# Kernel tuning notes

Measured on AMD Instinct MI355X. Metric: run time of the kernel, lower is better.

## Reference

```python
import jax, jax.numpy as jnp
import numpy as np

B, D = 4096, 512
STEPS = 50
LR, B1, B2, EPS = 0.01, 0.9, 0.999, 1e-8  # torch.optim.Adam defaults with lr=0.01


def setup_inputs() -> dict:
    key = jax.random.key(0)
    k1, k2, k3, k4 = jax.random.split(key, 4)
    s = jax.random.normal(k1, (B, D), dtype=jnp.float32)
    target_confidence = jax.random.uniform(k2, (B, 1), dtype=jnp.float32)
    # nn.Linear(style_dim, 1) init: U(-1/sqrt(D), 1/sqrt(D))
    lim = 1.0 / np.sqrt(D)
    W = jax.random.uniform(k3, (1, D), dtype=jnp.float32, minval=-lim, maxval=lim)
    b = jax.random.uniform(k4, (1,), dtype=jnp.float32, minval=-lim, maxval=lim)
    return {"s": s, "target_confidence": target_confidence, "W": W, "b": b}


def reference(s, target_confidence, W, b):
    # loss(x) = mse(sigmoid(x W^T + b), t) + l1(x, s); grad taken w.r.t. x only.
    def loss_fn(x):
        p = jax.nn.sigmoid(x @ W.T + b)                      # [B, 1]
        mse = jnp.mean((p - target_confidence) ** 2)
        d = x - s
        # stop_gradient(sign) so d|d|/dx = sign(d), with sign(0) = 0 (matches torch l1_loss subgradient)
        l1 = jnp.mean(jax.lax.stop_gradient(jnp.sign(d)) * d)
        return mse + l1

    grad_fn = jax.grad(loss_fn)

    def adam_step(carry, _):
        x, m, v, t = carry
        g = grad_fn(x)
        t = t + 1.0
        m = B1 * m + (1.0 - B1) * g
        v = B2 * v + (1.0 - B2) * g * g
        m_hat = m / (1.0 - B1 ** t)
        v_hat = v / (1.0 - B2 ** t)
        x = x - LR * m_hat / (jnp.sqrt(v_hat) + EPS)
        return (x, m, v, t), None

    init = (s, jnp.zeros_like(s), jnp.zeros_like(s), jnp.float32(0.0))
    (adjusted_s, _, _, _), _ = jax.lax.scan(adam_step, init, None, length=STEPS)
    return adjusted_s
```

## Files before the change

### kernel.cpp

```cpp
#include <hip/hip_runtime.h>

#define B_ 4096
#define D_ 512
#define STEPS_ 50

struct BcTab { float An[STEPS_]; };

#define DPP_ADD(x, ctrl) \
    ((x) + __int_as_float(__builtin_amdgcn_update_dpp( \
        0, __float_as_int(x), (ctrl), 0xf, 0xf, true)))

__device__ __forceinline__ float wave64_sum(float x) {
    x = DPP_ADD(x, 0x111);
    x = DPP_ADD(x, 0x112);
    x = DPP_ADD(x, 0x114);
    x = DPP_ADD(x, 0x118);
    x = DPP_ADD(x, 0x142);
    x = DPP_ADD(x, 0x143);
    return __int_as_float(__builtin_amdgcn_readlane(__float_as_int(x), 63));
}

__device__ __forceinline__ float sgn_l1(float d) {
    return __uint_as_float((__float_as_uint(d) & 0x80000000u) | 0x35000000u);
}

__device__ __forceinline__ float coef_from_z(float z, float t) {
    const float e = __expf(-z);
    const float q = __builtin_amdgcn_rcpf(1.0f + e);
    return (q - t) * (e * (q * q));
}

__global__ __launch_bounds__(64, 1) void adam_rows_kernel(
    const float* __restrict__ s,
    const float* __restrict__ tgt,
    const float* __restrict__ W,
    const float* __restrict__ bias_p,
    float* __restrict__ out,
    const BcTab bc)
{
    const int lane = threadIdx.x;
    const int r0 = blockIdx.x * 2;
    const int r1 = r0 + 1;

    const float4* s0 = (const float4*)(s + (size_t)r0 * D_);
    const float4* s1 = (const float4*)(s + (size_t)r1 * D_);
    const float4* W4 = (const float4*)W;

    float4 sa0 = s0[lane], sb0 = s0[lane + 64];
    float4 sa1 = s1[lane], sb1 = s1[lane + 64];
    float4 wa  = W4[lane], wb  = W4[lane + 64];
    const float t0 = tgt[r0], t1 = tgt[r1];
    const float b  = bias_p[0];

    const float c_mse = 2.0f / (float)B_;
    const float K     = (float)B_ * 0.5f;

    float2 ws[4] = {{wa.x * c_mse, wa.y * c_mse}, {wa.z * c_mse, wa.w * c_mse},
                    {wb.x * c_mse, wb.y * c_mse}, {wb.z * c_mse, wb.w * c_mse}};
    float2 ss0[4] = {{sa0.x, sa0.y}, {sa0.z, sa0.w}, {sb0.x, sb0.y}, {sb0.z, sb0.w}};
    float2 ss1[4] = {{sa1.x, sa1.y}, {sa1.z, sa1.w}, {sb1.x, sb1.y}, {sb1.z, sb1.w}};
    float2 dl0[4], dl1[4], M0[4], M1[4], V0[4], V1[4];

    float za0 = 0.0f, za1 = 0.0f;
#pragma unroll
    for (int j = 0; j < 4; ++j) {
        za0 = fmaf(ss0[j].x, ws[j].x, za0); za0 = fmaf(ss0[j].y, ws[j].y, za0);
        za1 = fmaf(ss1[j].x, ws[j].x, za1); za1 = fmaf(ss1[j].y, ws[j].y, za1);
    }
    const float zb0 = fmaf(K, wave64_sum(za0), b);
    const float zb1 = fmaf(K, wave64_sum(za1), b);

    float du0, du1;

    {
        const float c0 = coef_from_z(zb0, t0);
        const float c1 = coef_from_z(zb1, t1);
        const float An = bc.An[0];
        float a0 = 0.0f, a1 = 0.0f;
#pragma unroll
        for (int j = 0; j < 4; ++j) {
#pragma unroll
            for (int h = 0; h < 2; ++h) {
                float* w_  = h ? &ws[j].y  : &ws[j].x;
                float* m0_ = h ? &M0[j].y  : &M0[j].x;
                float* v0_ = h ? &V0[j].y  : &V0[j].x;
                float* d0_ = h ? &dl0[j].y : &dl0[j].x;
                float* m1_ = h ? &M1[j].y  : &M1[j].x;
                float* v1_ = h ? &V1[j].y  : &V1[j].x;
                float* d1_ = h ? &dl1[j].y : &dl1[j].x;
                const float g0 = c0 * *w_;
                const float g1 = c1 * *w_;
                *m0_ = g0; *v0_ = g0 * g0;
                *m1_ = g1; *v1_ = g1 * g1;
                const float r0r = __builtin_amdgcn_rsqf(fmaxf(*v0_, 1e-37f));
                const float r1r = __builtin_amdgcn_rsqf(fmaxf(*v1_, 1e-37f));
                *d0_ = (An * *m0_) * r0r;
                *d1_ = (An * *m1_) * r1r;
                a0 = fmaf(*d0_, *w_, a0);
                a1 = fmaf(*d1_, *w_, a1);
            }
        }
        du0 = a0; du1 = a1;
    }

#pragma unroll 1
    for (int step = 1; step < STEPS_; ++step) {
        const float z0 = fmaf(K, wave64_sum(du0), zb0);
        const float z1 = fmaf(K, wave64_sum(du1), zb1);
        const float c0 = coef_from_z(z0, t0);
        const float c1 = coef_from_z(z1, t1);
        const float An = bc.An[step];

        float a0 = 0.0f, a1 = 0.0f;
#pragma unroll
        for (int j = 0; j < 4; ++j) {
#pragma unroll
            for (int h = 0; h < 2; ++h) {
                float* w_  = h ? &ws[j].y  : &ws[j].x;
                float* m0_ = h ? &M0[j].y  : &M0[j].x;
                float* v0_ = h ? &V0[j].y  : &V0[j].x;
                float* d0_ = h ? &dl0[j].y : &dl0[j].x;
                float* m1_ = h ? &M1[j].y  : &M1[j].x;
                float* v1_ = h ? &V1[j].y  : &V1[j].x;
                float* d1_ = h ? &dl1[j].y : &dl1[j].x;
                const float g0 = fmaf(c0, *w_, sgn_l1(*d0_));
                const float g1 = fmaf(c1, *w_, sgn_l1(*d1_));
                *m0_ = fmaf(0.9f, *m0_, g0);
                *m1_ = fmaf(0.9f, *m1_, g1);
                *v0_ = fmaf(0.999f, *v0_, g0 * g0);
                *v1_ = fmaf(0.999f, *v1_, g1 * g1);
                const float r0r = __builtin_amdgcn_rsqf(fmaxf(*v0_, 1e-37f));
                const float r1r = __builtin_amdgcn_rsqf(fmaxf(*v1_, 1e-37f));
                *d0_ = fmaf(An * *m0_, r0r, *d0_);
                *d1_ = fmaf(An * *m1_, r1r, *d1_);
                a0 = fmaf(*d0_, *w_, a0);
                a1 = fmaf(*d1_, *w_, a1);
            }
        }
        du0 = a0; du1 = a1;
    }

    float4 oa0 = {ss0[0].x + dl0[0].x, ss0[0].y + dl0[0].y,
                  ss0[1].x + dl0[1].x, ss0[1].y + dl0[1].y};
    float4 ob0 = {ss0[2].x + dl0[2].x, ss0[2].y + dl0[2].y,
                  ss0[3].x + dl0[3].x, ss0[3].y + dl0[3].y};
    float4 oa1 = {ss1[0].x + dl1[0].x, ss1[0].y + dl1[0].y,
                  ss1[1].x + dl1[1].x, ss1[1].y + dl1[1].y};
    float4 ob1 = {ss1[2].x + dl1[2].x, ss1[2].y + dl1[2].y,
                  ss1[3].x + dl1[3].x, ss1[3].y + dl1[3].y};
    float4* o0 = (float4*)(out + (size_t)r0 * D_);
    float4* o1 = (float4*)(out + (size_t)r1 * D_);
    o0[lane] = oa0; o0[lane + 64] = ob0;
    o1[lane] = oa1; o1[lane + 64] = ob1;
}

extern "C" void kernel_launch(void* const* d_in, const int* in_sizes, int n_in,
                              void* d_out, int out_size, void* d_ws, size_t ws_size,
                              hipStream_t stream) {
    const float* s    = (const float*)d_in[0];
    const float* tgt  = (const float*)d_in[1];
    const float* W    = (const float*)d_in[2];
    const float* bias = (const float*)d_in[3];
    float* out = (float*)d_out;

    BcTab bc;
    double p1 = 1.0, p2 = 1.0;
    for (int t = 0; t < STEPS_; ++t) {
        p1 *= 0.9; p2 *= 0.999;
        bc.An[t] = (float)((-0.001 / (1.0 - p1)) /
                           __builtin_sqrt(0.001 / (1.0 - p2)));
    }

    adam_rows_kernel<<<dim3(B_ / 2), dim3(64), 0, stream>>>(s, tgt, W, bias, out, bc);
}
```

Baseline: 96.66 us.

## Skew two-row Adam recurrence so each row's reduction overlaps the other's update

Restructures the per-step loop so row 0's cross-lane reduction and sigmoid coefficient are computed while row 1's element update runs, staggering the two serial dependency chains instead of reducing both at the top of each step. It also replaces the fmax clamp with an epsilon folded into the v initialisation, uses copysign for the L1 sign term, and reloads s at the end instead of keeping it in registers across the loop. The aim is to hide DPP reduction and transcendental latency in a single-wave, latency-bound kernel. It risks small numerical differences from the epsilon change and adds global reloads at the end.

```diff
diff --git a/kernel.cpp b/kernel.cpp
--- a/kernel.cpp
+++ b/kernel.cpp
@@ -18,10 +18,6 @@
     x = DPP_ADD(x, 0x142);
     x = DPP_ADD(x, 0x143);
     return __int_as_float(__builtin_amdgcn_readlane(__float_as_int(x), 63));
-}
-
-__device__ __forceinline__ float sgn_l1(float d) {
-    return __uint_as_float((__float_as_uint(d) & 0x80000000u) | 0x35000000u);
 }
 
 __device__ __forceinline__ float coef_from_z(float z, float t) {
@@ -46,29 +42,34 @@
     const float4* s1 = (const float4*)(s + (size_t)r1 * D_);
     const float4* W4 = (const float4*)W;
 
-    float4 sa0 = s0[lane], sb0 = s0[lane + 64];
-    float4 sa1 = s1[lane], sb1 = s1[lane + 64];
-    float4 wa  = W4[lane], wb  = W4[lane + 64];
+    const float4 wa = W4[lane], wb = W4[lane + 64];
     const float t0 = tgt[r0], t1 = tgt[r1];
     const float b  = bias_p[0];
 
-    const float c_mse = 2.0f / (float)B_;
-    const float K     = (float)B_ * 0.5f;
+    const float c_mse = 0x1p-11f;
+    const float K     = 2048.0f;
+    const float c_l1  = 0x1p-21f;
 
-    float2 ws[4] = {{wa.x * c_mse, wa.y * c_mse}, {wa.z * c_mse, wa.w * c_mse},
-                    {wb.x * c_mse, wb.y * c_mse}, {wb.z * c_mse, wb.w * c_mse}};
-    float2 ss0[4] = {{sa0.x, sa0.y}, {sa0.z, sa0.w}, {sb0.x, sb0.y}, {sb0.z, sb0.w}};
-    float2 ss1[4] = {{sa1.x, sa1.y}, {sa1.z, sa1.w}, {sb1.x, sb1.y}, {sb1.z, sb1.w}};
-    float2 dl0[4], dl1[4], M0[4], M1[4], V0[4], V1[4];
+    float ws[8] = {wa.x * c_mse, wa.y * c_mse, wa.z * c_mse, wa.w * c_mse,
+                   wb.x * c_mse, wb.y * c_mse, wb.z * c_mse, wb.w * c_mse};
 
-    float za0 = 0.0f, za1 = 0.0f;
+    float dl0[8], dl1[8], M0[8], M1[8], V0[8], V1[8];
+
+    float zb0, zb1;
+    {
+        const float4 sa0 = s0[lane], sb0 = s0[lane + 64];
+        const float4 sa1 = s1[lane], sb1 = s1[lane + 64];
+        const float e0[8] = {sa0.x, sa0.y, sa0.z, sa0.w, sb0.x, sb0.y, sb0.z, sb0.w};
+        const float e1[8] = {sa1.x, sa1.y, sa1.z, sa1.w, sb1.x, sb1.y, sb1.z, sb1.w};
+        float za0 = 0.0f, za1 = 0.0f;
 #pragma unroll
-    for (int j = 0; j < 4; ++j) {
-        za0 = fmaf(ss0[j].x, ws[j].x, za0); za0 = fmaf(ss0[j].y, ws[j].y, za0);
-        za1 = fmaf(ss1[j].x, ws[j].x, za1); za1 = fmaf(ss1[j].y, ws[j].y, za1);
+        for (int k = 0; k < 8; ++k) {
+            za0 = fmaf(e0[k], ws[k], za0);
+            za1 = fmaf(e1[k], ws[k], za1);
+        }
+        zb0 = fmaf(K, wave64_sum(za0), b);
+        zb1 = fmaf(K, wave64_sum(za1), b);
     }
-    const float zb0 = fmaf(K, wave64_sum(za0), b);
-    const float zb1 = fmaf(K, wave64_sum(za1), b);
 
     float du0, du1;
 
@@ -78,80 +79,64 @@
         const float An = bc.An[0];
         float a0 = 0.0f, a1 = 0.0f;
 #pragma unroll
-        for (int j = 0; j < 4; ++j) {
-#pragma unroll
-            for (int h = 0; h < 2; ++h) {
-                float* w_  = h ? &ws[j].y  : &ws[j].x;
-                float* m0_ = h ? &M0[j].y  : &M0[j].x;
-                float* v0_ = h ? &V0[j].y  : &V0[j].x;
-                float* d0_ = h ? &dl0[j].y : &dl0[j].x;
-                float* m1_ = h ? &M1[j].y  : &M1[j].x;
-                float* v1_ = h ? &V1[j].y  : &V1[j].x;
-                float* d1_ = h ? &dl1[j].y : &dl1[j].x;
-                const float g0 = c0 * *w_;
-                const float g1 = c1 * *w_;
-                *m0_ = g0; *v0_ = g0 * g0;
-                *m1_ = g1; *v1_ = g1 * g1;
-                const float r0r = __builtin_amdgcn_rsqf(fmaxf(*v0_, 1e-37f));
-                const float r1r = __builtin_amdgcn_rsqf(fmaxf(*v1_, 1e-37f));
-                *d0_ = (An * *m0_) * r0r;
-                *d1_ = (An * *m1_) * r1r;
-                a0 = fmaf(*d0_, *w_, a0);
-                a1 = fmaf(*d1_, *w_, a1);
-            }
+        for (int k = 0; k < 8; ++k) {
+            const float g0 = c0 * ws[k];
+            const float g1 = c1 * ws[k];
+            M0[k] = g0;  V0[k] = fmaf(g0, g0, 1e-30f);
+            M1[k] = g1;  V1[k] = fmaf(g1, g1, 1e-30f);
+            dl0[k] = (An * M0[k]) * __builtin_amdgcn_rsqf(V0[k]);
+            dl1[k] = (An * M1[k]) * __builtin_amdgcn_rsqf(V1[k]);
+            a0 = fmaf(dl0[k], ws[k], a0);
+            a1 = fmaf(dl1[k], ws[k], a1);
         }
         du0 = a0; du1 = a1;
     }
 
+    float c0 = coef_from_z(fmaf(K, wave64_sum(du0), zb0), t0);
+
 #pragma unroll 1
     for (int step = 1; step < STEPS_; ++step) {
-        const float z0 = fmaf(K, wave64_sum(du0), zb0);
-        const float z1 = fmaf(K, wave64_sum(du1), zb1);
-        const float c0 = coef_from_z(z0, t0);
-        const float c1 = coef_from_z(z1, t1);
         const float An = bc.An[step];
 
-        float a0 = 0.0f, a1 = 0.0f;
+        const float c1 = coef_from_z(fmaf(K, wave64_sum(du1), zb1), t1);
+
+        float a0 = 0.0f;
 #pragma unroll
-        for (int j = 0; j < 4; ++j) {
+        for (int k = 0; k < 8; ++k) {
+            const float g = fmaf(c0, ws[k], __builtin_copysignf(c_l1, dl0[k]));
+            M0[k] = fmaf(0.9f,   M0[k], g);
+            V0[k] = fmaf(0.999f, V0[k], g * g);
+            dl0[k] = fmaf(An * M0[k], __builtin_amdgcn_rsqf(V0[k]), dl0[k]);
+            a0 = fmaf(dl0[k], ws[k], a0);
+        }
+        du0 = a0;
+
+        c0 = coef_from_z(fmaf(K, wave64_sum(du0), zb0), t0);
+
+        float a1 = 0.0f;
 #pragma unroll
-            for (int h = 0; h < 2; ++h) {
-                float* w_  = h ? &ws[j].y  : &ws[j].x;
-                float* m0_ = h ? &M0[j].y  : &M0[j].x;
-                float* v0_ = h ? &V0[j].y  : &V0[j].x;
-                float* d0_ = h ? &dl0[j].y : &dl0[j].x;
-                float* m1_ = h ? &M1[j].y  : &M1[j].x;
-                float* v1_ = h ? &V1[j].y  : &V1[j].x;
-                float* d1_ = h ? &dl1[j].y : &dl1[j].x;
-                const float g0 = fmaf(c0, *w_, sgn_l1(*d0_));
-                const float g1 = fmaf(c1, *w_, sgn_l1(*d1_));
-                *m0_ = fmaf(0.9f, *m0_, g0);
-                *m1_ = fmaf(0.9f, *m1_, g1);
-                *v0_ = fmaf(0.999f, *v0_, g0 * g0);
-                *v1_ = fmaf(0.999f, *v1_, g1 * g1);
-                const float r0r = __builtin_amdgcn_rsqf(fmaxf(*v0_, 1e-37f));
-                const float r1r = __builtin_amdgcn_rsqf(fmaxf(*v1_, 1e-37f));
-                *d0_ = fmaf(An * *m0_, r0r, *d0_);
-                *d1_ = fmaf(An * *m1_, r1r, *d1_);
-                a0 = fmaf(*d0_, *w_, a0);
-                a1 = fmaf(*d1_, *w_, a1);
-            }
+        for (int k = 0; k < 8; ++k) {
+            const float g = fmaf(c1, ws[k], __builtin_copysignf(c_l1, dl1[k]));
+            M1[k] = fmaf(0.9f,   M1[k], g);
+            V1[k] = fmaf(0.999f, V1[k], g * g);
+            dl1[k] = fmaf(An * M1[k], __builtin_amdgcn_rsqf(V1[k]), dl1[k]);
+            a1 = fmaf(dl1[k], ws[k], a1);
         }
-        du0 = a0; du1 = a1;
+        du1 = a1;
     }
 
-    float4 oa0 = {ss0[0].x + dl0[0].x, ss0[0].y + dl0[0].y,
-                  ss0[1].x + dl0[1].x, ss0[1].y + dl0[1].y};
-    float4 ob0 = {ss0[2].x + dl0[2].x, ss0[2].y + dl0[2].y,
-                  ss0[3].x + dl0[3].x, ss0[3].y + dl0[3].y};
-    float4 oa1 = {ss1[0].x + dl1[0].x, ss1[0].y + dl1[0].y,
-                  ss1[1].x + dl1[1].x, ss1[1].y + dl1[1].y};
-    float4 ob1 = {ss1[2].x + dl1[2].x, ss1[2].y + dl1[2].y,
-                  ss1[3].x + dl1[3].x, ss1[3].y + dl1[3].y};
-    float4* o0 = (float4*)(out + (size_t)r0 * D_);
-    float4* o1 = (float4*)(out + (size_t)r1 * D_);
-    o0[lane] = oa0; o0[lane + 64] = ob0;
-    o1[lane] = oa1; o1[lane + 64] = ob1;
+    {
+        const float4 sa0 = s0[lane], sb0 = s0[lane + 64];
+        const float4 sa1 = s1[lane], sb1 = s1[lane + 64];
+        float4 oa0 = {sa0.x + dl0[0], sa0.y + dl0[1], sa0.z + dl0[2], sa0.w + dl0[3]};
+        float4 ob0 = {sb0.x + dl0[4], sb0.y + dl0[5], sb0.z + dl0[6], sb0.w + dl0[7]};
+        float4 oa1 = {sa1.x + dl1[0], sa1.y + dl1[1], sa1.z + dl1[2], sa1.w + dl1[3]};
+        float4 ob1 = {sb1.x + dl1[4], sb1.y + dl1[5], sb1.z + dl1[6], sb1.w + dl1[7]};
+        float4* o0 = (float4*)(out + (size_t)r0 * D_);
+        float4* o1 = (float4*)(out + (size_t)r1 * D_);
+        o0[lane] = oa0; o0[lane + 64] = ob0;
+        o1[lane] = oa1; o1[lane + 64] = ob1;
+    }
 }
 
 extern "C" void kernel_launch(void* const* d_in, const int* in_sizes, int n_in,
```

Measured after the change: 93.07 us. -3.7%, faster.
